# Kernel optimization log

Hardware: AMD Instinct MI355X
Metric: run time of the kernel (lower is better)

Reference implementation:

```python
import jax, jax.numpy as jnp
import numpy as np

N = 10000
IN_DIM = 256
HID = 256
HEADS = 8
NUM_CLASSES = 40
EPS = 1e-5
NEG_SLOPE = 0.2


def gat_conv(x, src, dst, W, a_src, a_dst, bias, concat):
    # x: [N, F_in]; W: [F_in, H*C]; a_src/a_dst: [H, C]
    n = x.shape[0]
    H, C = a_src.shape
    h = (x @ W).reshape(n, H, C)                       # [N,H,C]
    s_src = jnp.einsum('nhc,hc->nh', h, a_src)         # [N,H]
    s_dst = jnp.einsum('nhc,hc->nh', h, a_dst)         # [N,H]
    score = jax.nn.leaky_relu(s_src[src] + s_dst[dst], NEG_SLOPE)  # [E,H]
    m = jax.lax.stop_gradient(jax.ops.segment_max(score, dst, num_segments=n))
    e = jnp.exp(score - m[dst])                        # [E,H]
    denom = jax.ops.segment_sum(e, dst, num_segments=n)
    alpha = e / denom[dst]                             # per-dst edge softmax
    msg = h[src] * alpha[:, :, None]                   # [E,H,C]
    out = jax.ops.segment_sum(msg, dst, num_segments=n)  # [N,H,C]
    out = out.reshape(n, H * C) if concat else out.mean(axis=1)
    return out + bias


def batch_norm(x, gamma, beta):
    mu = x.mean(axis=0)
    var = x.var(axis=0)
    return gamma * (x - mu) * jax.lax.rsqrt(var + EPS) + beta


def setup_inputs() -> dict:
    key = jax.random.key(0)
    ks = jax.random.split(key, 16)
    C0 = HID // HEADS  # 32, concat layer
    x = jax.random.normal(ks[0], (N, IN_DIM), jnp.float32)
    edge_index = jax.random.randint(ks[1], (2, 160000), 0, N, jnp.int32)
    def lin(k, fi, fo):
        return jax.random.normal(k, (fi, fo), jnp.float32) / np.sqrt(fi)
    return {
        'x': x,
        'edge_index': edge_index,
        'W0': lin(ks[2], IN_DIM, HEADS * C0),
        'a_src0': jax.random.normal(ks[3], (HEADS, C0), jnp.float32) * 0.1,
        'a_dst0': jax.random.normal(ks[4], (HEADS, C0), jnp.float32) * 0.1,
        'b0': jnp.zeros((HID,), jnp.float32),
        'g0': jnp.ones((HID,), jnp.float32),
        'be0': jnp.zeros((HID,), jnp.float32),
        'W1': lin(ks[5], HID, HEADS * HID),
        'a_src1': jax.random.normal(ks[6], (HEADS, HID), jnp.float32) * 0.1,
        'a_dst1': jax.random.normal(ks[7], (HEADS, HID), jnp.float32) * 0.1,
        'b1': jnp.zeros((HID,), jnp.float32),
        'g1': jnp.ones((HID,), jnp.float32),
        'be1': jnp.zeros((HID,), jnp.float32),
        'Wc': lin(ks[8], HID, NUM_CLASSES),
        'bc': jnp.zeros((NUM_CLASSES,), jnp.float32),
    }


def reference(x, edge_index, W0, a_src0, a_dst0, b0, g0, be0,
              W1, a_src1, a_dst1, b1, g1, be1, Wc, bc):
    n = x.shape[0]
    loops = jnp.arange(n, dtype=edge_index.dtype)
    src = jnp.concatenate([edge_index[0], loops])  # add_self_loops=True
    dst = jnp.concatenate([edge_index[1], loops])

    # layer 0: concat=True -> [N, 256]
    h = gat_conv(x, src, dst, W0, a_src0, a_dst0, b0, concat=True)
    h = jax.nn.elu(batch_norm(h, g0, be0))
    # i==0: no residual; dropout is identity at eval

    # layer 1 (last): concat=False (mean over heads) -> [N, 256]
    h_in = h
    h = gat_conv(h, src, dst, W1, a_src1, a_dst1, b1, concat=False)
    h = jax.nn.elu(batch_norm(h, g1, be1)) + h_in  # residual for i>0

    return h @ Wc + bc  # logits [N, num_classes]
```

## Files before the change

### kernel.cpp

```cpp
#include <hip/hip_runtime.h>
#include <math.h>

#define NN 10000
#define HEADS 8
#define NCLS 40
#define CHK 64
#define LOG2E 1.4426950408889634f

typedef __attribute__((ext_vector_type(8))) short short8;
typedef __attribute__((ext_vector_type(8))) unsigned short ushort8v;
typedef __attribute__((ext_vector_type(4))) float floatx4;

static __device__ __forceinline__ short f2bf(float f) {
    unsigned u = __builtin_bit_cast(unsigned, f);
    unsigned r = (u + 0x7fff + ((u >> 16) & 1)) >> 16;
    return (short)r;
}
static __device__ __forceinline__ float bf2f(unsigned short u) {
    unsigned x = ((unsigned)u) << 16;
    return __builtin_bit_cast(float, x);
}
static __device__ __forceinline__ void gl2lds16(const void* g, void* l) {
    __builtin_amdgcn_global_load_lds(
        (const __attribute__((address_space(1))) unsigned int*)g,
        (__attribute__((address_space(3))) unsigned int*)l, 16, 0, 0);
}

__global__ __launch_bounds__(256) void gemm_bf16_w128(
    const short* __restrict__ A, const short* __restrict__ Bt,
    float* __restrict__ C, short* __restrict__ Cbf,
    float* __restrict__ stats,
    const float* __restrict__ asrc, const float* __restrict__ adst,
    float* __restrict__ s0,
    const int* __restrict__ esrc, const int* __restrict__ edst,
    int* __restrict__ cursor, int* __restrict__ elist, int E, int scatBlocks,
    const float* __restrict__ W1, const float* __restrict__ a_src1,
    const float* __restrict__ a_dst1, float* __restrict__ v1,
    short* __restrict__ W1pT,
    int gemmBlocks, int gridY,
    int M, int Nn, int K, float alpha)
{
    __shared__ short As[2][64 * 64];
    __shared__ short Bs[2][128 * 64];
    const int tid = threadIdx.x;
    if ((int)blockIdx.x >= gemmBlocks) {
        int td = (int)blockIdx.x - gemmBlocks;
        if (td < scatBlocks) {
            int e = td * 256 + tid;
            if (e < E) {
                int dn = edst[e];
                int pos = atomicAdd(&cursor[dn], 1);
                elist[pos] = esrc[e];
            }
            return;
        }
        td -= scatBlocks;
        if (td < 16) {
            int idx = td * 256 + tid;
            int f = idx >> 4, j = idx & 15;
            int h = j & 7;
            const float* a = (j < 8) ? a_src1 : a_dst1;
            float s = 0.f;
            for (int c = 0; c < 256; c++)
                s += W1[f * 2048 + h * 256 + c] * a[h * 256 + c];
            v1[idx] = s;
            return;
        }
        td -= 16;
        {
            float (*tile)[33] = (float(*)[33])&As[0][0];
            int h = td >> 6, f0 = ((td >> 3) & 7) * 32, c0 = (td & 7) * 32;
            int tx = tid & 31, ty = tid >> 5;
            for (int r = ty; r < 32; r += 8)
                tile[r][tx] = W1[(size_t)(f0 + r) * 2048 + h * 256 + c0 + tx];
            __syncthreads();
            for (int r = ty; r < 32; r += 8)
                W1pT[(size_t)(c0 + r) * 2048 + h * 256 + f0 + tx] = f2bf(tile[tx][r]);
            return;
        }
    }
    const int w = tid >> 6, L = tid & 63;
    const int quad = L >> 4, lr = L & 15;
    const int d = blockIdx.x;
    const int by = (d >> 4) * 8 + (d & 7);
    const int bx = (d >> 3) & 1;
    if (by >= gridY) return;
    const int col0 = bx * 128, row0 = by * 64;

    const int schunk = (L & 7) ^ (L >> 3);
    const int sarow = w * 16 + (L >> 3);
    int ga0 = row0 + sarow;     if (ga0 > M - 1) ga0 = M - 1;
    int ga1 = row0 + sarow + 8; if (ga1 > M - 1) ga1 = M - 1;
    const short* agp0 = A + (size_t)ga0 * K + schunk * 8;
    const short* agp1 = A + (size_t)ga1 * K + schunk * 8;
    const int sbrow = w * 32 + (L >> 3);
    int gb[4];
    #pragma unroll
    for (int c = 0; c < 4; c++) {
        gb[c] = col0 + sbrow + c * 8;
        if (gb[c] > Nn - 1) gb[c] = Nn - 1;
    }
    const short* bgp0 = Bt + (size_t)gb[0] * K + schunk * 8;
    const short* bgp1 = Bt + (size_t)gb[1] * K + schunk * 8;
    const short* bgp2 = Bt + (size_t)gb[2] * K + schunk * 8;
    const short* bgp3 = Bt + (size_t)gb[3] * K + schunk * 8;

    floatx4 acc[4][2];
    const floatx4 zf = {0.f, 0.f, 0.f, 0.f};
    #pragma unroll
    for (int i = 0; i < 4; i++)
        #pragma unroll
        for (int j = 0; j < 2; j++) acc[i][j] = zf;

    const int nt = K >> 6;
    gl2lds16(agp0, &As[0][w * 1024]);
    gl2lds16(agp1, &As[0][w * 1024 + 512]);
    gl2lds16(bgp0, &Bs[0][w * 2048]);
    gl2lds16(bgp1, &Bs[0][w * 2048 + 512]);
    gl2lds16(bgp2, &Bs[0][w * 2048 + 1024]);
    gl2lds16(bgp3, &Bs[0][w * 2048 + 1536]);
    __syncthreads();
    int cur = 0;
    for (int t = 0; t < nt; t++) {
        if (t + 1 < nt) {
            const int k0 = (t + 1) << 6;
            const int nb = cur ^ 1;
            gl2lds16(agp0 + k0, &As[nb][w * 1024]);
            gl2lds16(agp1 + k0, &As[nb][w * 1024 + 512]);
            gl2lds16(bgp0 + k0, &Bs[nb][w * 2048]);
            gl2lds16(bgp1 + k0, &Bs[nb][w * 2048 + 512]);
            gl2lds16(bgp2 + k0, &Bs[nb][w * 2048 + 1024]);
            gl2lds16(bgp3 + k0, &Bs[nb][w * 2048 + 1536]);
        }
        #pragma unroll
        for (int ks = 0; ks < 2; ks++) {
            const int sl = ((ks * 4 + quad) ^ (lr & 7)) * 8;
            short8 bfr[2];
            #pragma unroll
            for (int j = 0; j < 2; j++)
                bfr[j] = *(const short8*)&Bs[cur][(w * 32 + j * 16 + lr) * 64 + sl];
            #pragma unroll
            for (int i = 0; i < 4; i++) {
                short8 afr = *(const short8*)&As[cur][(i * 16 + lr) * 64 + sl];
                #pragma unroll
                for (int j = 0; j < 2; j++)
                    acc[i][j] = __builtin_amdgcn_mfma_f32_16x16x32_bf16(afr, bfr[j], acc[i][j], 0, 0, 0);
            }
        }
        __syncthreads();
        cur ^= 1;
    }
    float s[2] = {0.f, 0.f}, s2[2] = {0.f, 0.f};
    #pragma unroll
    for (int j = 0; j < 2; j++) {
        int ccol = col0 + w * 32 + j * 16 + lr;
        if (ccol >= Nn) continue;
        #pragma unroll
        for (int i = 0; i < 4; i++) {
            #pragma unroll
            for (int r = 0; r < 4; r++) {
                int crow = row0 + i * 16 + quad * 4 + r;
                if (crow < M) {
                    float v = alpha * acc[i][j][r];
                    if (C)   C[(size_t)crow * Nn + ccol] = v;
                    if (Cbf) Cbf[(size_t)crow * Nn + ccol] = f2bf(v);
                    s[j] += v; s2[j] += v * v;
                }
            }
        }
    }
    if (stats) {
        #pragma unroll
        for (int j = 0; j < 2; j++) {
            s[j]  += __shfl_xor(s[j], 16, 64);  s[j]  += __shfl_xor(s[j], 32, 64);
            s2[j] += __shfl_xor(s2[j], 16, 64); s2[j] += __shfl_xor(s2[j], 32, 64);
        }
        if (L < 16) {
            #pragma unroll
            for (int j = 0; j < 2; j++) {
                int ccol = col0 + w * 32 + j * 16 + L;
                if (ccol < Nn) {
                    atomicAdd(&stats[ccol], s[j]);
                    atomicAdd(&stats[256 + ccol], s2[j]);
                }
            }
        }
    }
    if (s0) {
        const int head = bx * 4 + w;
        float as0 = asrc[col0 + w * 32 + lr];
        float as1 = asrc[col0 + w * 32 + 16 + lr];
        float ad0 = adst[col0 + w * 32 + lr];
        float ad1 = adst[col0 + w * 32 + 16 + lr];
        #pragma unroll
        for (int i = 0; i < 4; i++) {
            #pragma unroll
            for (int r = 0; r < 4; r++) {
                float ps = acc[i][0][r] * as0 + acc[i][1][r] * as1;
                float pd = acc[i][0][r] * ad0 + acc[i][1][r] * ad1;
                #pragma unroll
                for (int off = 1; off < 16; off <<= 1) {
                    ps += __shfl_xor(ps, off, 64);
                    pd += __shfl_xor(pd, off, 64);
                }
                if (lr == 0) {
                    int crow = row0 + i * 16 + quad * 4 + r;
                    if (crow < M) {
                        s0[crow * 16 + head] = alpha * ps;
                        s0[crow * 16 + 8 + head] = alpha * pd;
                    }
                }
            }
        }
    }
}

__global__ __launch_bounds__(256) void classifier_fused(
    const float* __restrict__ X, const float* __restrict__ stats,
    const float* __restrict__ g, const float* __restrict__ be,
    const unsigned short* __restrict__ resid,
    const short* __restrict__ Bt, float* __restrict__ C,
    const float* __restrict__ bias, int M, int Nn, int K)
{
    __shared__ short As[2][32 * 64];
    __shared__ short Bs[2][64 * 64];
    const int tid = threadIdx.x;
    const int w = tid >> 6, L = tid & 63;
    const int quad = L >> 4, lr = L & 15;
    const int row0 = blockIdx.x * 32;

    const int schunk = (L & 7) ^ (L >> 3);
    int ga = row0 + w * 8 + (L >> 3); if (ga > M - 1) ga = M - 1;
    int gbrow = w * 16 + (L >> 3);
    int gb0 = gbrow;     if (gb0 > Nn - 1) gb0 = Nn - 1;
    int gb1 = gbrow + 8; if (gb1 > Nn - 1) gb1 = Nn - 1;
    const float* xg = X + (size_t)ga * K + schunk * 8;
    const unsigned short* rg = resid + (size_t)ga * K + schunk * 8;
    const short* bgp0 = Bt + (size_t)gb0 * K + schunk * 8;
    const short* bgp1 = Bt + (size_t)gb1 * K + schunk * 8;

    floatx4 acc[2];
    const floatx4 zf = {0.f, 0.f, 0.f, 0.f};
    acc[0] = zf; acc[1] = zf;
    const float invN = 1.0f / NN;
    const int nt = K >> 6;

    floatx4 xa, xb2; ushort8v rv;
    xa  = *(const floatx4*)(xg);
    xb2 = *(const floatx4*)(xg + 4);
    rv  = *(const ushort8v*)(rg);
    gl2lds16(bgp0, &Bs[0][w * 1024]);
    gl2lds16(bgp1, &Bs[0][w * 1024 + 512]);
    {
        const int c = schunk * 8;
        short8 av;
        #pragma unroll
        for (int q = 0; q < 8; q++) {
            float m  = stats[c + q] * invN;
            float sq = stats[256 + c + q] * invN;
            float rs = rsqrtf(sq - m * m + 1e-5f) * g[c + q];
            float sh = be[c + q] - m * rs;
            float v = (q < 4 ? xa[q & 3] : xb2[q & 3]) * rs + sh;
            v = (v > 0.f) ? v : (expf(v) - 1.f);
            v += bf2f(rv[q]);
            av[q] = f2bf(v);
        }
        *(short8*)&As[0][w * 512 + L * 8] = av;
    }
    __syncthreads();
    int cur = 0;
    for (int t = 0; t < nt; t++) {
        floatx4 nxa, nxb2; ushort8v nrv;
        if (t + 1 < nt) {
            const int k0 = (t + 1) << 6;
            nxa  = *(const floatx4*)(xg + k0);
            nxb2 = *(const floatx4*)(xg + k0 + 4);
            nrv  = *(const ushort8v*)(rg + k0);
            gl2lds16(bgp0 + k0, &Bs[cur ^ 1][w * 1024]);
            gl2lds16(bgp1 + k0, &Bs[cur ^ 1][w * 1024 + 512]);
        }
        #pragma unroll
        for (int ks = 0; ks < 2; ks++) {
            const int sl = ((ks * 4 + quad) ^ (lr & 7)) * 8;
            short8 bfr = *(const short8*)&Bs[cur][(w * 16 + lr) * 64 + sl];
            #pragma unroll
            for (int i = 0; i < 2; i++) {
                short8 afr = *(const short8*)&As[cur][(i * 16 + lr) * 64 + sl];
                acc[i] = __builtin_amdgcn_mfma_f32_16x16x32_bf16(afr, bfr, acc[i], 0, 0, 0);
            }
        }
        if (t + 1 < nt) {
            const int c = schunk * 8 + ((t + 1) << 6);
            short8 av;
            #pragma unroll
            for (int q = 0; q < 8; q++) {
                float m  = stats[c + q] * invN;
                float sq = stats[256 + c + q] * invN;
                float rs = rsqrtf(sq - m * m + 1e-5f) * g[c + q];
                float sh = be[c + q] - m * rs;
                float v = (q < 4 ? nxa[q & 3] : nxb2[q & 3]) * rs + sh;
                v = (v > 0.f) ? v : (expf(v) - 1.f);
                v += bf2f(nrv[q]);
                av[q] = f2bf(v);
            }
            *(short8*)&As[cur ^ 1][w * 512 + L * 8] = av;
        }
        __syncthreads();
        cur ^= 1;
    }
    const int ccol = w * 16 + lr;
    if (ccol < Nn) {
        float bv = bias ? bias[ccol] : 0.f;
        #pragma unroll
        for (int i = 0; i < 2; i++) {
            #pragma unroll
            for (int r = 0; r < 4; r++) {
                int crow = row0 + i * 16 + quad * 4 + r;
                if (crow < M) C[(size_t)crow * Nn + ccol] = acc[i][r] + bv;
            }
        }
    }
}

__global__ __launch_bounds__(256) void prep_a(
    const float* __restrict__ x, const float* __restrict__ W0,
    const float* __restrict__ Wc, const int* __restrict__ edst, int E,
    short* __restrict__ xb, short* __restrict__ W0T, short* __restrict__ WcT,
    int* __restrict__ counts)
{
    const int b = blockIdx.x, t = threadIdx.x;
    if (b < 2500) {
        int i = b * 256 + t;
        floatx4 v = ((const floatx4*)x)[i];
        short4 o = {f2bf(v[0]), f2bf(v[1]), f2bf(v[2]), f2bf(v[3])};
        ((short4*)xb)[i] = o;
    } else if (b < 2756) {
        int o = b - 2500;
        W0T[o * 256 + t] = f2bf(W0[t * 256 + o]);
    } else if (b < 2796) {
        int o = b - 2756;
        WcT[o * 256 + t] = f2bf(Wc[t * 40 + o]);
    } else {
        int e = (b - 2796) * 256 + t;
        if (e < E) atomicAdd(&counts[edst[e]], 1);
    }
}

__global__ __launch_bounds__(1024) void scan_kernel(
    int* __restrict__ counts, int* __restrict__ offsets,
    int* __restrict__ cursor, int* __restrict__ elist)
{
    __shared__ int wsum[16];
    const int t = threadIdx.x, lane = t & 63, wid = t >> 6;
    constexpr int P = 10;
    const int base = t * P;
    int deg[P], loc[P];
    int s = 0;
    #pragma unroll
    for (int j = 0; j < P; j++) {
        int i = base + j;
        loc[j] = s;
        deg[j] = (i < NN) ? counts[i] + 1 : 0;
        s += deg[j];
    }
    int inc = s;
    #pragma unroll
    for (int off = 1; off < 64; off <<= 1) {
        int tv = __shfl_up(inc, off, 64);
        if (lane >= off) inc += tv;
    }
    if (lane == 63) wsum[wid] = inc;
    __syncthreads();
    if (t < 16) {
        int v = wsum[t];
        int winc = v;
        #pragma unroll
        for (int off = 1; off < 16; off <<= 1) {
            int tv = __shfl_up(winc, off, 16);
            if (t >= off) winc += tv;
        }
        wsum[t] = winc - v;
    }
    __syncthreads();
    int excl = inc - s + wsum[wid];
    #pragma unroll
    for (int j = 0; j < P; j++) {
        int i = base + j;
        if (i < NN) {
            int o = excl + loc[j];
            counts[i] = deg[j];
            offsets[i] = o;
            elist[o] = i;
            cursor[i] = o + 1;
        }
    }
}

__global__ __launch_bounds__(256) void agg0_fused(
    const unsigned short* __restrict__ h0b, const float* __restrict__ s0,
    const int* __restrict__ offsets, const int* __restrict__ counts,
    const int* __restrict__ elist, float* __restrict__ out)
{
    __shared__ float pw_s[4][CHK * 8];
    __shared__ int   sn_s[4][CHK];
    const int wid = threadIdx.x >> 6, L = threadIdx.x & 63;
    const int n = blockIdx.x * 4 + wid;
    float* pw = pw_s[wid];
    int*   sw = sn_s[wid];
    const int deg = counts[n], start = offsets[n];
    const int hL = L >> 3;

    floatx4 sda = *(const floatx4*)(s0 + n * 16 + 8);
    floatx4 sdb = *(const floatx4*)(s0 + n * 16 + 12);
    float sd[8] = {sda[0], sda[1], sda[2], sda[3], sdb[0], sdb[1], sdb[2], sdb[3]};
    float lp[8] = {0.f, 0.f, 0.f, 0.f, 0.f, 0.f, 0.f, 0.f};
    float a0 = 0.f, a1 = 0.f, a2 = 0.f, a3 = 0.f;

    for (int e0 = 0; e0 < deg; e0 += CHK) {
        int ch = deg - e0; if (ch > CHK) ch = CHK;
        if (L < ch) {
            int sn = elist[start + e0 + L];
            sw[L] = sn;
            floatx4 ssa = *(const floatx4*)(s0 + sn * 16);
            floatx4 ssb = *(const floatx4*)(s0 + sn * 16 + 4);
            float ss[8] = {ssa[0], ssa[1], ssa[2], ssa[3], ssb[0], ssb[1], ssb[2], ssb[3]};
            float p[8];
            #pragma unroll
            for (int h = 0; h < 8; h++) {
                float v = ss[h] + sd[h];
                v = (v > 0.f) ? v : 0.2f * v;
                p[h] = exp2f(v * LOG2E);
                lp[h] += p[h];
            }
            floatx4 p0 = {p[0], p[1], p[2], p[3]};
            floatx4 p1 = {p[4], p[5], p[6], p[7]};
            *(floatx4*)&pw[L * 8] = p0;
            *(floatx4*)&pw[L * 8 + 4] = p1;
        }
        int e = 0;
        for (; e + 2 <= ch; e += 2) {
            float wA = pw[e * 8 + hL];
            float wB = pw[e * 8 + 8 + hL];
            ushort4 vA = *(const ushort4*)(h0b + (size_t)sw[e] * 256 + 4 * L);
            ushort4 vB = *(const ushort4*)(h0b + (size_t)sw[e + 1] * 256 + 4 * L);
            a0 += wA * bf2f(vA.x); a1 += wA * bf2f(vA.y);
            a2 += wA * bf2f(vA.z); a3 += wA * bf2f(vA.w);
            a0 += wB * bf2f(vB.x); a1 += wB * bf2f(vB.y);
            a2 += wB * bf2f(vB.z); a3 += wB * bf2f(vB.w);
        }
        if (e < ch) {
            float wA = pw[e * 8 + hL];
            ushort4 vA = *(const ushort4*)(h0b + (size_t)sw[e] * 256 + 4 * L);
            a0 += wA * bf2f(vA.x); a1 += wA * bf2f(vA.y);
            a2 += wA * bf2f(vA.z); a3 += wA * bf2f(vA.w);
        }
    }
    #pragma unroll
    for (int off = 1; off < 64; off <<= 1)
        #pragma unroll
        for (int h = 0; h < 8; h++)
            lp[h] += __shfl_xor(lp[h], off, 64);
    float inv = 1.f / lp[hL];
    floatx4 o = {a0 * inv, a1 * inv, a2 * inv, a3 * inv};
    *(floatx4*)(out + (size_t)n * 256 + 4 * L) = o;
}

__global__ __launch_bounds__(256) void agg1_full(
    const unsigned short* __restrict__ hb, const float* __restrict__ s1,
    const int* __restrict__ offsets, const int* __restrict__ counts,
    const int* __restrict__ elist, short* __restrict__ aggout)
{
    __shared__ float pw_s[4][CHK * 8];
    __shared__ int   sn_s[4][CHK];
    const int wid = threadIdx.x >> 6, L = threadIdx.x & 63;
    const int n = blockIdx.x * 4 + wid;
    float* pw = pw_s[wid];
    int*   sw = sn_s[wid];
    const int deg = counts[n], start = offsets[n];

    floatx4 sda = *(const floatx4*)(s1 + n * 16 + 8);
    floatx4 sdb = *(const floatx4*)(s1 + n * 16 + 12);
    float sd[8] = {sda[0], sda[1], sda[2], sda[3], sdb[0], sdb[1], sdb[2], sdb[3]};
    float lp[8] = {0.f, 0.f, 0.f, 0.f, 0.f, 0.f, 0.f, 0.f};
    float acc[8][4];
    #pragma unroll
    for (int h = 0; h < 8; h++)
        #pragma unroll
        for (int f = 0; f < 4; f++) acc[h][f] = 0.f;

    for (int e0 = 0; e0 < deg; e0 += CHK) {
        int ch = deg - e0; if (ch > CHK) ch = CHK;
        if (L < ch) {
            int sn = elist[start + e0 + L];
            sw[L] = sn;
            floatx4 ssa = *(const floatx4*)(s1 + sn * 16);
            floatx4 ssb = *(const floatx4*)(s1 + sn * 16 + 4);
            float ss[8] = {ssa[0], ssa[1], ssa[2], ssa[3], ssb[0], ssb[1], ssb[2], ssb[3]};
            float p[8];
            #pragma unroll
            for (int h = 0; h < 8; h++) {
                float v = ss[h] + sd[h];
                v = (v > 0.f) ? v : 0.2f * v;
                p[h] = exp2f(v * LOG2E);
                lp[h] += p[h];
            }
            floatx4 p0 = {p[0], p[1], p[2], p[3]};
            floatx4 p1 = {p[4], p[5], p[6], p[7]};
            *(floatx4*)&pw[L * 8] = p0;
            *(floatx4*)&pw[L * 8 + 4] = p1;
        }
        int e = 0;
        for (; e + 2 <= ch; e += 2) {
            floatx4 p0A = *(const floatx4*)&pw[e * 8];
            floatx4 p1A = *(const floatx4*)&pw[e * 8 + 4];
            floatx4 p0B = *(const floatx4*)&pw[e * 8 + 8];
            floatx4 p1B = *(const floatx4*)&pw[e * 8 + 12];
            ushort4 vA = *(const ushort4*)(hb + (size_t)sw[e] * 256 + 4 * L);
            ushort4 vB = *(const ushort4*)(hb + (size_t)sw[e + 1] * 256 + 4 * L);
            float a0 = bf2f(vA.x), a1 = bf2f(vA.y), a2 = bf2f(vA.z), a3 = bf2f(vA.w);
            float b0 = bf2f(vB.x), b1 = bf2f(vB.y), b2 = bf2f(vB.z), b3 = bf2f(vB.w);
            #pragma unroll
            for (int h = 0; h < 4; h++) {
                acc[h][0] += p0A[h] * a0;     acc[h][1] += p0A[h] * a1;
                acc[h][2] += p0A[h] * a2;     acc[h][3] += p0A[h] * a3;
                acc[h + 4][0] += p1A[h] * a0; acc[h + 4][1] += p1A[h] * a1;
                acc[h + 4][2] += p1A[h] * a2; acc[h + 4][3] += p1A[h] * a3;
            }
            #pragma unroll
            for (int h = 0; h < 4; h++) {
                acc[h][0] += p0B[h] * b0;     acc[h][1] += p0B[h] * b1;
                acc[h][2] += p0B[h] * b2;     acc[h][3] += p0B[h] * b3;
                acc[h + 4][0] += p1B[h] * b0; acc[h + 4][1] += p1B[h] * b1;
                acc[h + 4][2] += p1B[h] * b2; acc[h + 4][3] += p1B[h] * b3;
            }
        }
        if (e < ch) {
            floatx4 p0A = *(const floatx4*)&pw[e * 8];
            floatx4 p1A = *(const floatx4*)&pw[e * 8 + 4];
            ushort4 vA = *(const ushort4*)(hb + (size_t)sw[e] * 256 + 4 * L);
            float a0 = bf2f(vA.x), a1 = bf2f(vA.y), a2 = bf2f(vA.z), a3 = bf2f(vA.w);
            #pragma unroll
            for (int h = 0; h < 4; h++) {
                acc[h][0] += p0A[h] * a0;     acc[h][1] += p0A[h] * a1;
                acc[h][2] += p0A[h] * a2;     acc[h][3] += p0A[h] * a3;
                acc[h + 4][0] += p1A[h] * a0; acc[h + 4][1] += p1A[h] * a1;
                acc[h + 4][2] += p1A[h] * a2; acc[h + 4][3] += p1A[h] * a3;
            }
        }
    }
    #pragma unroll
    for (int off = 1; off < 64; off <<= 1)
        #pragma unroll
        for (int h = 0; h < 8; h++)
            lp[h] += __shfl_xor(lp[h], off, 64);
    #pragma unroll
    for (int h = 0; h < 8; h++) {
        float inv = 1.f / lp[h];
        short4 o = {f2bf(acc[h][0] * inv), f2bf(acc[h][1] * inv),
                    f2bf(acc[h][2] * inv), f2bf(acc[h][3] * inv)};
        *(short4*)(aggout + (size_t)n * 2048 + h * 256 + 4 * L) = o;
    }
}

__global__ __launch_bounds__(1024) void bn_stats_kernel(
    const float* __restrict__ x, float* __restrict__ stats, int n)
{
    __shared__ float red[16][512];
    const int t = threadIdx.x;
    const int sub = t >> 6, c4 = (t & 63) * 4;
    floatx4 s = {0.f, 0.f, 0.f, 0.f}, s2 = {0.f, 0.f, 0.f, 0.f};
    for (int r = blockIdx.x * 16 + sub; r < n; r += gridDim.x * 16) {
        floatx4 v = *(const floatx4*)(x + (size_t)r * 256 + c4);
        s += v; s2 += v * v;
    }
    #pragma unroll
    for (int k = 0; k < 4; k++) {
        red[sub][c4 + k] = s[k];
        red[sub][256 + c4 + k] = s2[k];
    }
    __syncthreads();
    if (t < 512) {
        float acc = 0.f;
        #pragma unroll
        for (int i = 0; i < 16; i++) acc += red[i][t];
        atomicAdd(&stats[t], acc);
    }
}

__global__ __launch_bounds__(256) void bnapply_score1(
    const float* __restrict__ xg, const float* __restrict__ stats,
    const float* __restrict__ g, const float* __restrict__ be,
    const float* __restrict__ v1, short* __restrict__ hactb, float* __restrict__ s1)
{
    __shared__ float row[256];
    __shared__ float part[16][17];
    const int n = blockIdx.x, t = threadIdx.x;
    const float invN = 1.0f / NN;
    float mu = stats[t] * invN;
    float var = stats[256 + t] * invN - mu * mu;
    float v = g[t] * (xg[(size_t)n * 256 + t] - mu) * rsqrtf(var + 1e-5f) + be[t];
    v = (v > 0.f) ? v : (expf(v) - 1.f);
    hactb[(size_t)n * 256 + t] = f2bf(v);
    row[t] = v;
    __syncthreads();
    int j = t & 15, f0 = t >> 4;
    float p = 0.f;
    #pragma unroll
    for (int k = 0; k < 16; k++)
        p += row[f0 * 16 + k] * v1[(f0 * 16 + k) * 16 + j];
    part[f0][j] = p;
    __syncthreads();
    if (t < 16) {
        float s = 0.f;
        #pragma unroll
        for (int k = 0; k < 16; k++) s += part[k][t];
        s1[n * 16 + t] = s;
    }
}

extern "C" void kernel_launch(void* const* d_in, const int* in_sizes, int n_in,
                              void* d_out, int out_size, void* d_ws, size_t ws_size,
                              hipStream_t stream) {
    const float* x      = (const float*)d_in[0];
    const int*   eidx   = (const int*)d_in[1];
    const float* W0     = (const float*)d_in[2];
    const float* a_src0 = (const float*)d_in[3];
    const float* a_dst0 = (const float*)d_in[4];
    const float* g0     = (const float*)d_in[6];
    const float* be0    = (const float*)d_in[7];
    const float* W1     = (const float*)d_in[8];
    const float* a_src1 = (const float*)d_in[9];
    const float* a_dst1 = (const float*)d_in[10];
    const float* g1     = (const float*)d_in[12];
    const float* be1    = (const float*)d_in[13];
    const float* Wc     = (const float*)d_in[14];
    const float* bc     = (const float*)d_in[15];
    float* out = (float*)d_out;

    const int E = in_sizes[1] / 2;
    const int* esrc = eidx;
    const int* edst = eidx + E;

    char* ws = (char*)d_ws;
    size_t off = 0;
    auto alloc = [&](size_t bytes) {
        void* p = ws + off;
        off += (bytes + 255) & ~(size_t)255;
        return p;
    };
    float* stats   = (float*)alloc(1024 * 4);
    int*   counts  = (int*)alloc(NN * 4);
    float* out1    = (float*)alloc((size_t)NN * 256 * 4);
    short* h0b     = (short*)alloc((size_t)NN * 256 * 2);
    short* xb      = (short*)alloc((size_t)NN * 256 * 2);
    float* s0      = (float*)alloc((size_t)NN * 16 * 4);
    float* s1      = (float*)alloc((size_t)NN * 16 * 4);
    float* v1      = (float*)alloc(4096 * 4);
    float* h_gat0  = (float*)alloc((size_t)NN * 256 * 4);
    short* hactb   = (short*)alloc((size_t)NN * 256 * 2);
    short* agg1bf  = (short*)alloc((size_t)NN * 2048 * 2);
    short* W0T     = (short*)alloc((size_t)256 * 256 * 2);
    short* W1pT    = (short*)alloc((size_t)256 * 2048 * 2);
    short* WcT     = (short*)alloc((size_t)64 * 256 * 2);
    int* offsets   = (int*)alloc((NN + 16) * 4);
    int* cursor    = (int*)alloc(NN * 4);
    int* elist     = (int*)alloc((size_t)(E + NN) * 4);

    float* stats0 = stats;
    float* stats1 = stats + 512;

    hipMemsetAsync(stats, 0, 1024 * 4 + NN * 4, stream);

    const int cntBlocks = (E + 255) / 256;

    prep_a<<<2796 + cntBlocks, 256, 0, stream>>>(
        x, W0, Wc, edst, E, xb, W0T, WcT, counts);

    scan_kernel<<<1, 1024, 0, stream>>>(counts, offsets, cursor, elist);

    const int gy = (NN + 63) / 64;
    const int gB = 16 * ((gy + 7) / 8);

    gemm_bf16_w128<<<gB + cntBlocks + 528, 256, 0, stream>>>(
        xb, W0T, nullptr, h0b, nullptr,
        a_src0, a_dst0, s0,
        esrc, edst, cursor, elist, E, cntBlocks,
        W1, a_src1, a_dst1, v1, W1pT,
        gB, gy, NN, 256, 256, 1.0f);

    agg0_fused<<<NN / 4, 256, 0, stream>>>(
        (const unsigned short*)h0b, s0, offsets, counts, elist, h_gat0);
    bn_stats_kernel<<<64, 1024, 0, stream>>>(h_gat0, stats0, NN);
    bnapply_score1<<<NN, 256, 0, stream>>>(h_gat0, stats0, g0, be0, v1, hactb, s1);

    agg1_full<<<NN / 4, 256, 0, stream>>>(
        (const unsigned short*)hactb, s1, offsets, counts, elist, agg1bf);
    gemm_bf16_w128<<<gB, 256, 0, stream>>>(
        agg1bf, W1pT, out1, nullptr, stats1,
        nullptr, nullptr, nullptr,
        nullptr, nullptr, nullptr, nullptr, 0, 0,
        nullptr, nullptr, nullptr, nullptr, nullptr,
        gB, gy, NN, 256, 2048, 0.125f);

    classifier_fused<<<(NN + 31) / 32, 256, 0, stream>>>(
        out1, stats1, g1, be1, (const unsigned short*)hactb,
        WcT, out, bc, NN, NCLS, 256);
}
```

Baseline: 248.3 us.

## Fuse fp32-to-bf16 conversion of x into GEMM A-tile load, single-buffer LDS

```diff
diff --git a/kernel.cpp b/kernel.cpp
--- a/kernel.cpp
+++ b/kernel.cpp
@@ -27,7 +27,8 @@
 }
 
 __global__ __launch_bounds__(256) void gemm_bf16_w128(
-    const short* __restrict__ A, const short* __restrict__ Bt,
+    const float* __restrict__ Af32, const short* __restrict__ A,
+    const short* __restrict__ Bt,
     float* __restrict__ C, short* __restrict__ Cbf,
     float* __restrict__ stats,
     const float* __restrict__ asrc, const float* __restrict__ adst,
@@ -40,8 +41,8 @@
     int gemmBlocks, int gridY,
     int M, int Nn, int K, float alpha)
 {
-    __shared__ short As[2][64 * 64];
-    __shared__ short Bs[2][128 * 64];
+    __shared__ short As[64 * 64];
+    __shared__ short Bs[128 * 64];
     const int tid = threadIdx.x;
     if ((int)blockIdx.x >= gemmBlocks) {
         int td = (int)blockIdx.x - gemmBlocks;
@@ -68,7 +69,7 @@
         }
         td -= 16;
         {
-            float (*tile)[33] = (float(*)[33])&As[0][0];
+            float (*tile)[33] = (float(*)[33])As;
             int h = td >> 6, f0 = ((td >> 3) & 7) * 32, c0 = (td & 7) * 32;
             int tx = tid & 31, ty = tid >> 5;
             for (int r = ty; r < 32; r += 8)
@@ -91,8 +92,12 @@
     const int sarow = w * 16 + (L >> 3);
     int ga0 = row0 + sarow;     if (ga0 > M - 1) ga0 = M - 1;
     int ga1 = row0 + sarow + 8; if (ga1 > M - 1) ga1 = M - 1;
-    const short* agp0 = A + (size_t)ga0 * K + schunk * 8;
-    const short* agp1 = A + (size_t)ga1 * K + schunk * 8;
+    const short* agp0 = A    ? A    + (size_t)ga0 * K + schunk * 8 : nullptr;
+    const short* agp1 = A    ? A    + (size_t)ga1 * K + schunk * 8 : nullptr;
+    const float* axp0 = Af32 ? Af32 + (size_t)ga0 * K + schunk * 8 : nullptr;
+    const float* axp1 = Af32 ? Af32 + (size_t)ga1 * K + schunk * 8 : nullptr;
+    short* alw0 = &As[w * 1024 + L * 8];
+    short* alw1 = &As[w * 1024 + 512 + L * 8];
     const int sbrow = w * 32 + (L >> 3);
     int gb[4];
     #pragma unroll
@@ -104,6 +109,10 @@
     const short* bgp1 = Bt + (size_t)gb[1] * K + schunk * 8;
     const short* bgp2 = Bt + (size_t)gb[2] * K + schunk * 8;
     const short* bgp3 = Bt + (size_t)gb[3] * K + schunk * 8;
+    short* blp0 = &Bs[w * 2048];
+    short* blp1 = &Bs[w * 2048 + 512];
+    short* blp2 = &Bs[w * 2048 + 1024];
+    short* blp3 = &Bs[w * 2048 + 1536];
 
     floatx4 acc[4][2];
     const floatx4 zf = {0.f, 0.f, 0.f, 0.f};
@@ -112,43 +121,45 @@
         #pragma unroll
         for (int j = 0; j < 2; j++) acc[i][j] = zf;
 
-    const int nt = K >> 6;
-    gl2lds16(agp0, &As[0][w * 1024]);
-    gl2lds16(agp1, &As[0][w * 1024 + 512]);
-    gl2lds16(bgp0, &Bs[0][w * 2048]);
-    gl2lds16(bgp1, &Bs[0][w * 2048 + 512]);
-    gl2lds16(bgp2, &Bs[0][w * 2048 + 1024]);
-    gl2lds16(bgp3, &Bs[0][w * 2048 + 1536]);
-    __syncthreads();
-    int cur = 0;
-    for (int t = 0; t < nt; t++) {
-        if (t + 1 < nt) {
-            const int k0 = (t + 1) << 6;
-            const int nb = cur ^ 1;
-            gl2lds16(agp0 + k0, &As[nb][w * 1024]);
-            gl2lds16(agp1 + k0, &As[nb][w * 1024 + 512]);
-            gl2lds16(bgp0 + k0, &Bs[nb][w * 2048]);
-            gl2lds16(bgp1 + k0, &Bs[nb][w * 2048 + 512]);
-            gl2lds16(bgp2 + k0, &Bs[nb][w * 2048 + 1024]);
-            gl2lds16(bgp3 + k0, &Bs[nb][w * 2048 + 1536]);
-        }
+    for (int k0 = 0; k0 < K; k0 += 64) {
+        gl2lds16(bgp0 + k0, blp0);
+        gl2lds16(bgp1 + k0, blp1);
+        gl2lds16(bgp2 + k0, blp2);
+        gl2lds16(bgp3 + k0, blp3);
+        if (Af32) {
+            floatx4 va0 = *(const floatx4*)(axp0 + k0);
+            floatx4 va1 = *(const floatx4*)(axp0 + k0 + 4);
+            floatx4 vb0 = *(const floatx4*)(axp1 + k0);
+            floatx4 vb1 = *(const floatx4*)(axp1 + k0 + 4);
+            short8 o0, o1;
+            #pragma unroll
+            for (int q = 0; q < 8; q++) {
+                o0[q] = f2bf(q < 4 ? va0[q & 3] : va1[q & 3]);
+                o1[q] = f2bf(q < 4 ? vb0[q & 3] : vb1[q & 3]);
+            }
+            *(short8*)alw0 = o0;
+            *(short8*)alw1 = o1;
+        } else {
+            gl2lds16(agp0 + k0, &As[w * 1024]);
+            gl2lds16(agp1 + k0, &As[w * 1024 + 512]);
+        }
+        __syncthreads();
         #pragma unroll
         for (int ks = 0; ks < 2; ks++) {
             const int sl = ((ks * 4 + quad) ^ (lr & 7)) * 8;
             short8 bfr[2];
             #pragma unroll
             for (int j = 0; j < 2; j++)
-                bfr[j] = *(const short8*)&Bs[cur][(w * 32 + j * 16 + lr) * 64 + sl];
+                bfr[j] = *(const short8*)&Bs[(w * 32 + j * 16 + lr) * 64 + sl];
             #pragma unroll
             for (int i = 0; i < 4; i++) {
-                short8 afr = *(const short8*)&As[cur][(i * 16 + lr) * 64 + sl];
+                short8 afr = *(const short8*)&As[(i * 16 + lr) * 64 + sl];
                 #pragma unroll
                 for (int j = 0; j < 2; j++)
                     acc[i][j] = __builtin_amdgcn_mfma_f32_16x16x32_bf16(afr, bfr[j], acc[i][j], 0, 0, 0);
             }
         }
         __syncthreads();
-        cur ^= 1;
     }
     float s[2] = {0.f, 0.f}, s2[2] = {0.f, 0.f};
     #pragma unroll
@@ -323,25 +334,19 @@
 }
 
 __global__ __launch_bounds__(256) void prep_a(
-    const float* __restrict__ x, const float* __restrict__ W0,
-    const float* __restrict__ Wc, const int* __restrict__ edst, int E,
-    short* __restrict__ xb, short* __restrict__ W0T, short* __restrict__ WcT,
+    const float* __restrict__ W0, const float* __restrict__ Wc,
+    const int* __restrict__ edst, int E,
+    short* __restrict__ W0T, short* __restrict__ WcT,
     int* __restrict__ counts)
 {
     const int b = blockIdx.x, t = threadIdx.x;
-    if (b < 2500) {
-        int i = b * 256 + t;
-        floatx4 v = ((const floatx4*)x)[i];
-        short4 o = {f2bf(v[0]), f2bf(v[1]), f2bf(v[2]), f2bf(v[3])};
-        ((short4*)xb)[i] = o;
-    } else if (b < 2756) {
-        int o = b - 2500;
-        W0T[o * 256 + t] = f2bf(W0[t * 256 + o]);
-    } else if (b < 2796) {
-        int o = b - 2756;
+    if (b < 256) {
+        W0T[b * 256 + t] = f2bf(W0[t * 256 + b]);
+    } else if (b < 296) {
+        int o = b - 256;
         WcT[o * 256 + t] = f2bf(Wc[t * 40 + o]);
     } else {
-        int e = (b - 2796) * 256 + t;
+        int e = (b - 296) * 256 + t;
         if (e < E) atomicAdd(&counts[edst[e]], 1);
     }
 }
@@ -652,7 +657,6 @@
     int*   counts  = (int*)alloc(NN * 4);
     float* out1    = (float*)alloc((size_t)NN * 256 * 4);
     short* h0b     = (short*)alloc((size_t)NN * 256 * 2);
-    short* xb      = (short*)alloc((size_t)NN * 256 * 2);
     float* s0      = (float*)alloc((size_t)NN * 16 * 4);
     float* s1      = (float*)alloc((size_t)NN * 16 * 4);
     float* v1      = (float*)alloc(4096 * 4);
@@ -673,8 +677,7 @@
 
     const int cntBlocks = (E + 255) / 256;
 
-    prep_a<<<2796 + cntBlocks, 256, 0, stream>>>(
-        x, W0, Wc, edst, E, xb, W0T, WcT, counts);
+    prep_a<<<296 + cntBlocks, 256, 0, stream>>>(W0, Wc, edst, E, W0T, WcT, counts);
 
     scan_kernel<<<1, 1024, 0, stream>>>(counts, offsets, cursor, elist);
 
@@ -682,7 +685,7 @@
     const int gB = 16 * ((gy + 7) / 8);
 
     gemm_bf16_w128<<<gB + cntBlocks + 528, 256, 0, stream>>>(
-        xb, W0T, nullptr, h0b, nullptr,
+        x, nullptr, W0T, nullptr, h0b, nullptr,
         a_src0, a_dst0, s0,
         esrc, edst, cursor, elist, E, cntBlocks,
         W1, a_src1, a_dst1, v1, W1pT,
@@ -696,7 +699,7 @@
     agg1_full<<<NN / 4, 256, 0, stream>>>(
         (const unsigned short*)hactb, s1, offsets, counts, elist, agg1bf);
     gemm_bf16_w128<<<gB, 256, 0, stream>>>(
-        agg1bf, W1pT, out1, nullptr, stats1,
+        nullptr, agg1bf, W1pT, out1, nullptr, stats1,
         nullptr, nullptr, nullptr,
         nullptr, nullptr, nullptr, nullptr, 0, 0,
         nullptr, nullptr, nullptr, nullptr, nullptr,
```

After: 245.8 us. Within noise of the previous version (-1.0%).
